# Optimization experiments

Measured on AMD Instinct MI355X. Metric: run time of the kernel, lower is better.

The kernel has to match this reference:

```python
import jax, jax.numpy as jnp
import numpy as np

B, S, H, M = 8, 128, 768, 128
EPS = 1e-12


def setup_inputs() -> dict:
    key = jax.random.key(0)
    ks = jax.random.split(key, 8)
    seq_hiddens = jax.random.normal(ks[0], (B, S, H), dtype=jnp.float32)
    gamma = jnp.ones((H,), jnp.float32)
    beta = jnp.zeros((H,), jnp.float32)
    # conditional LN dense weights (torch Linear weight: (out, in)); small init so math stays stable
    w_beta = jax.random.normal(ks[1], (H, H), dtype=jnp.float32) * 0.02
    w_gamma = jax.random.normal(ks[2], (H, H), dtype=jnp.float32) * 0.02
    w_ent = jax.random.normal(ks[3], (H, M), dtype=jnp.float32) * 0.02
    w_head = jax.random.normal(ks[4], (H, M), dtype=jnp.float32) * 0.02
    w_tail = jax.random.normal(ks[5], (H, M), dtype=jnp.float32) * 0.02
    b_ent = jnp.zeros((M,), jnp.float32)
    b_head = jnp.zeros((M,), jnp.float32)
    b_tail = jnp.zeros((M,), jnp.float32)
    return dict(seq_hiddens=seq_hiddens, gamma=gamma, beta=beta, w_beta=w_beta,
                w_gamma=w_gamma, w_ent=w_ent, b_ent=b_ent, w_head=w_head,
                b_head=b_head, w_tail=w_tail, b_tail=b_tail)


def _handshake_cln(seq, gamma, beta, w_beta, w_gamma):
    # Triangular pair expansion in the same row-major order as the torch loop:
    # for ind in range(S): pairs (ind, ind), (ind, ind+1), ..., (ind, S-1)
    s = seq.shape[1]
    ii, jj = jnp.triu_indices(s)                 # (P,) each, P = S(S+1)/2
    x = seq[:, jj, :]                            # visible hiddens   (B, P, H)
    cond = seq[:, ii, :]                         # repeated hiddens  (B, P, H)
    beta_c = jnp.einsum('bph,oh->bpo', cond, w_beta) + beta      # (B, P, H)
    gamma_c = jnp.einsum('bph,oh->bpo', cond, w_gamma) + gamma   # (B, P, H)
    mean = jnp.mean(x, axis=-1, keepdims=True)
    out = x - mean
    var = jnp.mean(out * out, axis=-1, keepdims=True)
    std = (var + EPS) ** 2                       # NOTE: faithful to source (no sqrt)
    return out / std * gamma_c + beta_c


def reference(seq_hiddens, gamma, beta, w_beta, w_gamma, w_ent, b_ent,
              w_head, b_head, w_tail, b_tail):
    shaking = _handshake_cln(seq_hiddens, gamma, beta, w_beta, w_gamma)  # (B, P, H)
    ent = jnp.tanh(shaking @ w_ent + b_ent)      # (B, P, M)
    head = jnp.tanh(shaking @ w_head + b_head)
    tail = jnp.tanh(shaking @ w_tail + b_tail)
    return jnp.stack([ent, head, tail], axis=0)  # (3, B, P, M)
```

## Files before the change

kernel.cpp:

```cpp
#include <hip/hip_runtime.h>
#include <hip/hip_bf16.h>
#include <hip/hip_fp16.h>
#include <math.h>

#define B_   8
#define S_   128
#define H_   768
#define M_   128
#define P_   8256
#define BP_  66048
#define EPSF 1e-12f

typedef unsigned short u16;
typedef unsigned int   u32;
typedef _Float16 h16;
typedef _Float16 ffrag __attribute__((ext_vector_type(8)));
typedef float    f32x4 __attribute__((ext_vector_type(4)));

__device__ __forceinline__ u32 fuse2(u32 x, u32 g, u32 b) {
    __half2 r = __hfma2(__builtin_bit_cast(__half2, x),
                        __builtin_bit_cast(__half2, g),
                        __builtin_bit_cast(__half2, b));
    return __builtin_bit_cast(u32, r);
}
__device__ __forceinline__ float fast_tanh(float v) {
    float t = __expf(v + v);
    float r = __builtin_amdgcn_rcpf(t + 1.0f);
    return fmaf(-2.0f, r, 1.0f);
}
__device__ __forceinline__ void gl_lds16(const h16* g, h16* l) {
    __builtin_amdgcn_global_load_lds(
        (const __attribute__((address_space(1))) u32*)g,
        (__attribute__((address_space(3))) u32*)l, 16, 0, 0);
}

#define NORM0 5763
__global__ void k_prep(const float* __restrict__ seq,
                       const float* __restrict__ wg, const float* __restrict__ wb,
                       const float* __restrict__ we, const float* __restrict__ wh,
                       const float* __restrict__ wt,
                       const float* __restrict__ be, const float* __restrict__ bh,
                       const float* __restrict__ bt,
                       h16* __restrict__ wgb, h16* __restrict__ wbb,
                       h16* __restrict__ wpk, float* __restrict__ biasc,
                       h16* __restrict__ xn, h16* __restrict__ condb)
{
    __shared__ float red[4];
    const int bx = blockIdx.x;
    const int t = threadIdx.x;

    if (bx < NORM0) {
        int idx = bx * 256 + t;
        if (idx < 589824) {
            wgb[idx] = (h16)wg[idx];
        } else if (idx < 1179648) {
            int i = idx - 589824;
            wbb[i] = (h16)wb[i];
        } else if (idx < 1474560) {
            int i = idx - 1179648;
            int e  = i & 7;
            int n  = (i >> 3) & 127;
            int v  = i >> 10;
            int ch = v & 7;
            int w2 = v >> 3;
            int kt = w2 % 12;
            int nb = w2 / 12;
            int h  = kt * 64 + ch * 8 + e;
            const float* src = (nb == 0) ? we : (nb == 1 ? wh : wt);
            wpk[i] = (h16)src[h * 128 + n];
        } else if (idx < 1474944) {
            int n = idx - 1474560;
            biasc[n] = (n < 128) ? be[n] : (n < 256 ? bh[n - 128] : bt[n - 256]);
        }
        return;
    }
    const int row = bx - NORM0;
    const int lane = t & 63, wid = t >> 6;
    const float* x = seq + (size_t)row * H_;
    float x0 = x[t], x1 = x[t + 256], x2 = x[t + 512];

    float s = x0 + x1 + x2;
    for (int o = 32; o; o >>= 1) s += __shfl_xor(s, o);
    if (lane == 0) red[wid] = s;
    __syncthreads();
    float mean = (red[0] + red[1] + red[2] + red[3]) * (1.0f / 768.0f);

    float c0 = x0 - mean, c1 = x1 - mean, c2 = x2 - mean;
    float ss = c0 * c0 + c1 * c1 + c2 * c2;
    for (int o = 32; o; o >>= 1) ss += __shfl_xor(ss, o);
    __syncthreads();
    if (lane == 0) red[wid] = ss;
    __syncthreads();
    float var = (red[0] + red[1] + red[2] + red[3]) * (1.0f / 768.0f);
    float sd = var + EPSF;
    float scale = 1.0f / (sd * sd);

    h16* xr = xn + (size_t)row * H_;
    h16* cr = condb + (size_t)row * H_;
    xr[t] = (h16)(c0 * scale); xr[t + 256] = (h16)(c1 * scale); xr[t + 512] = (h16)(c2 * scale);
    cr[t] = (h16)x0;           cr[t + 256] = (h16)x1;           cr[t + 512] = (h16)x2;
}

__global__ __launch_bounds__(256) void k_cond_gemm(
    const h16* __restrict__ Ab, const h16* __restrict__ Wg, const h16* __restrict__ Wb,
    const float* __restrict__ gamma, const float* __restrict__ beta,
    h16* __restrict__ Gc, h16* __restrict__ Bc)
{
    __shared__ h16 Ash[64 * 72];
    __shared__ h16 Bsh[64 * 72];
    const int t = threadIdx.x;
    const int row0 = blockIdx.x * 64;
    const int by = blockIdx.y;
    const bool isg = (by < 12);
    const int nc0 = (isg ? by : by - 12) * 64;
    const h16* wsrc = isg ? Wg : Wb;

    const int r = t >> 2, q = t & 3;
    const h16* ap = Ab + (size_t)(row0 + r) * H_ + q * 16;
    const h16* wp = wsrc + (size_t)(nc0 + r) * H_ + q * 16;
    h16* asto = &Ash[r * 72 + q * 16];
    h16* bsto = &Bsh[r * 72 + q * 16];

    const int lane = t & 63, wid = t >> 6;
    const int wm0 = (wid >> 1) * 32, wn0 = (wid & 1) * 32;
    const int l15 = lane & 15, quad = lane >> 4, q8 = quad * 8;

    f32x4 acc[2][2] = {};
    for (int kt = 0; kt < 12; ++kt) {
        const int k0 = kt * 64;
        uint4 a0 = *(const uint4*)(ap + k0); uint4 a1 = *(const uint4*)(ap + k0 + 8);
        uint4 w0 = *(const uint4*)(wp + k0); uint4 w1 = *(const uint4*)(wp + k0 + 8);
        *(uint4*)asto = a0; *(uint4*)(asto + 8) = a1;
        *(uint4*)bsto = w0; *(uint4*)(bsto + 8) = w1;
        __syncthreads();
#pragma unroll
        for (int ks = 0; ks < 64; ks += 32) {
            ffrag af[2], bf[2];
#pragma unroll
            for (int mi = 0; mi < 2; ++mi)
                af[mi] = *reinterpret_cast<const ffrag*>(&Ash[(wm0 + mi * 16 + l15) * 72 + ks + q8]);
#pragma unroll
            for (int ni = 0; ni < 2; ++ni)
                bf[ni] = *reinterpret_cast<const ffrag*>(&Bsh[(wn0 + ni * 16 + l15) * 72 + ks + q8]);
#pragma unroll
            for (int mi = 0; mi < 2; ++mi)
#pragma unroll
                for (int ni = 0; ni < 2; ++ni)
                    acc[mi][ni] = __builtin_amdgcn_mfma_f32_16x16x32_f16(af[mi], bf[ni], acc[mi][ni], 0, 0, 0);
        }
        __syncthreads();
    }

    const float* bias = isg ? gamma : beta;
    h16* outp = isg ? Gc : Bc;
#pragma unroll
    for (int mi = 0; mi < 2; ++mi)
#pragma unroll
        for (int ni = 0; ni < 2; ++ni) {
            int c = wn0 + ni * 16 + l15;
            float bv = bias[nc0 + c];
#pragma unroll
            for (int reg = 0; reg < 4; ++reg) {
                int rg = wm0 + mi * 16 + quad * 4 + reg;
                outp[(size_t)(row0 + rg) * H_ + nc0 + c] = (h16)(acc[mi][ni][reg] + bv);
            }
        }
}

__global__ __launch_bounds__(256, 2) void k_pair_gemm(
    const h16* __restrict__ Xn, const h16* __restrict__ Gcb, const h16* __restrict__ Bcb,
    const h16* __restrict__ Wpk, const float* __restrict__ biasc,
    float* __restrict__ out)
{
    __shared__ h16 Ash[2][8 * 128 * 8];
    __shared__ h16 Bsh[2][8 * 128 * 8];

    const int t = threadIdx.x;
    const int row0 = blockIdx.x * 128;
    const int nb = blockIdx.y;

    const int r_s = t >> 1, half = t & 1;
    int gp = row0 + r_s;
    int b = gp / P_;
    int p = gp - b * P_;
    int i = (int)((257.0f - sqrtf(66049.0f - 8.0f * (float)p)) * 0.5f);
    if (i < 0) i = 0; if (i > 127) i = 127;
    while (i > 0 && (i * (257 - i)) / 2 > p) --i;
    while (((i + 1) * (256 - i)) / 2 <= p) ++i;
    int j = i + (p - (i * (257 - i)) / 2);

    const h16* xp  = Xn  + (size_t)(b * 128 + j) * H_ + half * 32;
    const h16* gp_ = Gcb + (size_t)(b * 128 + i) * H_ + half * 32;
    const h16* bp_ = Bcb + (size_t)(b * 128 + i) * H_ + half * 32;
    int aw[4];
#pragma unroll
    for (int u = 0; u < 4; ++u)
        aw[u] = ((half * 4 + u) * 128 + r_s) * 8;

    const h16* wtile = Wpk + (size_t)nb * 12 * 8192;
    const int wud = t & ~63;

    const int lane = t & 63, wid = t >> 6;
    const int wm0 = (wid >> 1) * 64, wn0 = (wid & 1) * 64;
    const int l15 = lane & 15, quad = lane >> 4;

#pragma unroll
    for (int c = 0; c < 4; ++c)
        gl_lds16(wtile + (size_t)(c * 256 + t) * 8, &Bsh[0][(c * 256 + wud) * 8]);
    {
        uint4 xa[4], ga[4], ba[4];
#pragma unroll
        for (int u = 0; u < 4; ++u) {
            xa[u] = *(const uint4*)(xp + u * 8);
            ga[u] = *(const uint4*)(gp_ + u * 8);
            ba[u] = *(const uint4*)(bp_ + u * 8);
        }
#pragma unroll
        for (int u = 0; u < 4; ++u) {
            uint4 f;
            f.x = fuse2(xa[u].x, ga[u].x, ba[u].x); f.y = fuse2(xa[u].y, ga[u].y, ba[u].y);
            f.z = fuse2(xa[u].z, ga[u].z, ba[u].z); f.w = fuse2(xa[u].w, ga[u].w, ba[u].w);
            *(uint4*)&Ash[0][aw[u]] = f;
        }
    }
    __syncthreads();

    f32x4 acc[4][4] = {};
#pragma unroll 2
    for (int kt = 0; kt < 12; ++kt) {
        const int buf = kt & 1, nbf = buf ^ 1;
        uint4 xa[4], ga[4], ba[4];
        if (kt < 11) {
            const h16* wnext = wtile + (size_t)(kt + 1) * 8192;
#pragma unroll
            for (int c = 0; c < 4; ++c)
                gl_lds16(wnext + (size_t)(c * 256 + t) * 8, &Bsh[nbf][(c * 256 + wud) * 8]);
            const int k0 = (kt + 1) * 64;
#pragma unroll
            for (int u = 0; u < 4; ++u) {
                xa[u] = *(const uint4*)(xp + k0 + u * 8);
                ga[u] = *(const uint4*)(gp_ + k0 + u * 8);
                ba[u] = *(const uint4*)(bp_ + k0 + u * 8);
            }
        }

#pragma unroll
        for (int ks = 0; ks < 64; ks += 32) {
            const int ch0 = ks >> 3;
            ffrag af[4], bf[4];
#pragma unroll
            for (int mi = 0; mi < 4; ++mi)
                af[mi] = *reinterpret_cast<const ffrag*>(
                    &Ash[buf][((ch0 + quad) * 128 + wm0 + mi * 16 + l15) * 8]);
#pragma unroll
            for (int ni = 0; ni < 4; ++ni)
                bf[ni] = *reinterpret_cast<const ffrag*>(
                    &Bsh[buf][((ch0 + quad) * 128 + wn0 + ni * 16 + l15) * 8]);
#pragma unroll
            for (int mi = 0; mi < 4; ++mi)
#pragma unroll
                for (int ni = 0; ni < 4; ++ni)
                    acc[mi][ni] = __builtin_amdgcn_mfma_f32_16x16x32_f16(af[mi], bf[ni], acc[mi][ni], 0, 0, 0);
        }

        if (kt < 11) {
#pragma unroll
            for (int u = 0; u < 4; ++u) {
                uint4 f;
                f.x = fuse2(xa[u].x, ga[u].x, ba[u].x); f.y = fuse2(xa[u].y, ga[u].y, ba[u].y);
                f.z = fuse2(xa[u].z, ga[u].z, ba[u].z); f.w = fuse2(xa[u].w, ga[u].w, ba[u].w);
                *(uint4*)&Ash[nbf][aw[u]] = f;
            }
        }
        __syncthreads();
    }

#pragma unroll
    for (int mi = 0; mi < 4; ++mi)
#pragma unroll
        for (int ni = 0; ni < 4; ++ni) {
            int c = wn0 + ni * 16 + l15;
            float bv = biasc[nb * 128 + c];
#pragma unroll
            for (int reg = 0; reg < 4; ++reg) {
                int rg = wm0 + mi * 16 + quad * 4 + reg;
                out[((size_t)nb * BP_ + row0 + rg) * M_ + c] = fast_tanh(acc[mi][ni][reg] + bv);
            }
        }
}

extern "C" void kernel_launch(void* const* d_in, const int* in_sizes, int n_in,
                              void* d_out, int out_size, void* d_ws, size_t ws_size,
                              hipStream_t stream)
{
    const float* seq     = (const float*)d_in[0];
    const float* gamma   = (const float*)d_in[1];
    const float* beta    = (const float*)d_in[2];
    const float* w_beta  = (const float*)d_in[3];
    const float* w_gamma = (const float*)d_in[4];
    const float* w_ent   = (const float*)d_in[5];
    const float* b_ent   = (const float*)d_in[6];
    const float* w_head  = (const float*)d_in[7];
    const float* b_head  = (const float*)d_in[8];
    const float* w_tail  = (const float*)d_in[9];
    const float* b_tail  = (const float*)d_in[10];
    float* out = (float*)d_out;

    char* ws = (char*)d_ws;
    h16* xn    = (h16*)ws; ws += (size_t)1024 * 768 * 2;
    h16* condb = (h16*)ws; ws += (size_t)1024 * 768 * 2;
    h16* wgb   = (h16*)ws; ws += (size_t)768 * 768 * 2;
    h16* wbb   = (h16*)ws; ws += (size_t)768 * 768 * 2;
    h16* wpk   = (h16*)ws; ws += (size_t)294912 * 2;
    h16* gc    = (h16*)ws; ws += (size_t)1024 * 768 * 2;
    h16* bc    = (h16*)ws; ws += (size_t)1024 * 768 * 2;
    float* biasc = (float*)ws; ws += 384 * 4;

    hipLaunchKernelGGL(k_prep, dim3(NORM0 + 1024), dim3(256), 0, stream,
                       seq, w_gamma, w_beta, w_ent, w_head, w_tail,
                       b_ent, b_head, b_tail, wgb, wbb, wpk, biasc, xn, condb);
    hipLaunchKernelGGL(k_cond_gemm, dim3(16, 24), dim3(256), 0, stream,
                       condb, wgb, wbb, gamma, beta, gc, bc);
    hipLaunchKernelGGL(k_pair_gemm, dim3(516, 3), dim3(256), 0, stream,
                       xn, gc, bc, wpk, biasc, out);
}
```

Baseline: 200.5 us.

## Triple-buffer weight tiles and prefetch activations two stages ahead

The weight tile in shared memory becomes a three-slot ring, so the global-to-LDS copy for stage kt+2 is issued while stage kt is being multiplied. The fused activation tile for the next stage is now written to LDS before the MFMA block. Its register loads run two stages ahead, which gives global latency more time to hide. The full __syncthreads is replaced by an LDS-count wait plus s_barrier, and sched_barrier and setprio hints are added around the MFMA section. LDS per block grows to 80KB, which may limit occupancy. The lighter barrier relies on the compiler to insert the vector-memory waits for the asynchronous LDS copies.

```diff
diff --git a/kernel.cpp b/kernel.cpp
--- a/kernel.cpp
+++ b/kernel.cpp
@@ -173,7 +173,7 @@
     float* __restrict__ out)
 {
     __shared__ h16 Ash[2][8 * 128 * 8];
-    __shared__ h16 Bsh[2][8 * 128 * 8];
+    __shared__ h16 Bsh[3][8 * 128 * 8];
 
     const int t = threadIdx.x;
     const int row0 = blockIdx.x * 128;
@@ -204,38 +204,59 @@
     const int wm0 = (wid >> 1) * 64, wn0 = (wid & 1) * 64;
     const int l15 = lane & 15, quad = lane >> 4;
 
+    uint4 xa[4], ga[4], ba[4];
+
+#pragma unroll
+    for (int u = 0; u < 4; ++u) {
+        xa[u] = *(const uint4*)(xp + u * 8);
+        ga[u] = *(const uint4*)(gp_ + u * 8);
+        ba[u] = *(const uint4*)(bp_ + u * 8);
+    }
+#pragma unroll
+    for (int u = 0; u < 4; ++u) {
+        uint4 f;
+        f.x = fuse2(xa[u].x, ga[u].x, ba[u].x); f.y = fuse2(xa[u].y, ga[u].y, ba[u].y);
+        f.z = fuse2(xa[u].z, ga[u].z, ba[u].z); f.w = fuse2(xa[u].w, ga[u].w, ba[u].w);
+        *(uint4*)&Ash[0][aw[u]] = f;
+    }
 #pragma unroll
     for (int c = 0; c < 4; ++c)
         gl_lds16(wtile + (size_t)(c * 256 + t) * 8, &Bsh[0][(c * 256 + wud) * 8]);
-    {
-        uint4 xa[4], ga[4], ba[4];
-#pragma unroll
-        for (int u = 0; u < 4; ++u) {
-            xa[u] = *(const uint4*)(xp + u * 8);
-            ga[u] = *(const uint4*)(gp_ + u * 8);
-            ba[u] = *(const uint4*)(bp_ + u * 8);
-        }
-#pragma unroll
-        for (int u = 0; u < 4; ++u) {
-            uint4 f;
-            f.x = fuse2(xa[u].x, ga[u].x, ba[u].x); f.y = fuse2(xa[u].y, ga[u].y, ba[u].y);
-            f.z = fuse2(xa[u].z, ga[u].z, ba[u].z); f.w = fuse2(xa[u].w, ga[u].w, ba[u].w);
-            *(uint4*)&Ash[0][aw[u]] = f;
-        }
-    }
-    __syncthreads();
+#pragma unroll
+    for (int c = 0; c < 4; ++c)
+        gl_lds16(wtile + 8192 + (size_t)(c * 256 + t) * 8, &Bsh[1][(c * 256 + wud) * 8]);
+    __builtin_amdgcn_sched_barrier(0);
+#pragma unroll
+    for (int u = 0; u < 4; ++u) {
+        xa[u] = *(const uint4*)(xp + 64 + u * 8);
+        ga[u] = *(const uint4*)(gp_ + 64 + u * 8);
+        ba[u] = *(const uint4*)(bp_ + 64 + u * 8);
+    }
+    asm volatile("s_waitcnt lgkmcnt(0)" ::: "memory");
+    __builtin_amdgcn_s_barrier();
 
     f32x4 acc[4][4] = {};
-#pragma unroll 2
+    int bcur = 0, bpre = 2;
     for (int kt = 0; kt < 12; ++kt) {
-        const int buf = kt & 1, nbf = buf ^ 1;
-        uint4 xa[4], ga[4], ba[4];
+        if (kt < 10) {
+            const h16* wnext = wtile + (size_t)(kt + 2) * 8192;
+#pragma unroll
+            for (int c = 0; c < 4; ++c)
+                gl_lds16(wnext + (size_t)(c * 256 + t) * 8, &Bsh[bpre][(c * 256 + wud) * 8]);
+        }
+        __builtin_amdgcn_sched_barrier(0);
         if (kt < 11) {
-            const h16* wnext = wtile + (size_t)(kt + 1) * 8192;
-#pragma unroll
-            for (int c = 0; c < 4; ++c)
-                gl_lds16(wnext + (size_t)(c * 256 + t) * 8, &Bsh[nbf][(c * 256 + wud) * 8]);
-            const int k0 = (kt + 1) * 64;
+            const int abn = (kt + 1) & 1;
+#pragma unroll
+            for (int u = 0; u < 4; ++u) {
+                uint4 f;
+                f.x = fuse2(xa[u].x, ga[u].x, ba[u].x); f.y = fuse2(xa[u].y, ga[u].y, ba[u].y);
+                f.z = fuse2(xa[u].z, ga[u].z, ba[u].z); f.w = fuse2(xa[u].w, ga[u].w, ba[u].w);
+                *(uint4*)&Ash[abn][aw[u]] = f;
+            }
+        }
+        if (kt < 10) {
+            const int k0 = (kt + 2) * 64;
 #pragma unroll
             for (int u = 0; u < 4; ++u) {
                 xa[u] = *(const uint4*)(xp + k0 + u * 8);
@@ -243,36 +264,36 @@
                 ba[u] = *(const uint4*)(bp_ + k0 + u * 8);
             }
         }
-
-#pragma unroll
-        for (int ks = 0; ks < 64; ks += 32) {
-            const int ch0 = ks >> 3;
-            ffrag af[4], bf[4];
-#pragma unroll
-            for (int mi = 0; mi < 4; ++mi)
-                af[mi] = *reinterpret_cast<const ffrag*>(
-                    &Ash[buf][((ch0 + quad) * 128 + wm0 + mi * 16 + l15) * 8]);
-#pragma unroll
-            for (int ni = 0; ni < 4; ++ni)
-                bf[ni] = *reinterpret_cast<const ffrag*>(
-                    &Bsh[buf][((ch0 + quad) * 128 + wn0 + ni * 16 + l15) * 8]);
-#pragma unroll
-            for (int mi = 0; mi < 4; ++mi)
+        __builtin_amdgcn_sched_barrier(0);
+        {
+            const int ab = kt & 1;
+            __builtin_amdgcn_s_setprio(1);
+#pragma unroll
+            for (int ks = 0; ks < 64; ks += 32) {
+                const int ch0 = ks >> 3;
+                ffrag af[4], bf[4];
+#pragma unroll
+                for (int mi = 0; mi < 4; ++mi)
+                    af[mi] = *reinterpret_cast<const ffrag*>(
+                        &Ash[ab][((ch0 + quad) * 128 + wm0 + mi * 16 + l15) * 8]);
 #pragma unroll
                 for (int ni = 0; ni < 4; ++ni)
-                    acc[mi][ni] = __builtin_amdgcn_mfma_f32_16x16x32_f16(af[mi], bf[ni], acc[mi][ni], 0, 0, 0);
-        }
-
+                    bf[ni] = *reinterpret_cast<const ffrag*>(
+                        &Bsh[bcur][((ch0 + quad) * 128 + wn0 + ni * 16 + l15) * 8]);
+#pragma unroll
+                for (int mi = 0; mi < 4; ++mi)
+#pragma unroll
+                    for (int ni = 0; ni < 4; ++ni)
+                        acc[mi][ni] = __builtin_amdgcn_mfma_f32_16x16x32_f16(af[mi], bf[ni], acc[mi][ni], 0, 0, 0);
+            }
+            __builtin_amdgcn_s_setprio(0);
+        }
+        bcur = (bcur == 2) ? 0 : bcur + 1;
+        bpre = (bpre == 2) ? 0 : bpre + 1;
         if (kt < 11) {
-#pragma unroll
-            for (int u = 0; u < 4; ++u) {
-                uint4 f;
-                f.x = fuse2(xa[u].x, ga[u].x, ba[u].x); f.y = fuse2(xa[u].y, ga[u].y, ba[u].y);
-                f.z = fuse2(xa[u].z, ga[u].z, ba[u].z); f.w = fuse2(xa[u].w, ga[u].w, ba[u].w);
-                *(uint4*)&Ash[nbf][aw[u]] = f;
-            }
-        }
-        __syncthreads();
+            asm volatile("s_waitcnt lgkmcnt(0)" ::: "memory");
+            __builtin_amdgcn_s_barrier();
+        }
     }
 
 #pragma unroll
```

Measured after the change: 204.1 us. Within noise of the previous version (+1.8%).

## Switch pair GEMM to 32x32x16 MFMA with 32-wide K tiles and higher occupancy

Applied to the files above, without the earlier changes.

The main pair GEMM now uses 32x32x16 MFMA instructions instead of 16x16x32. The K tile drops from 64 to 32, so the loop runs 24 steps instead of 12, and launch bounds rise to 4 blocks per CU. The packed weight layout and LDS buffers are resized to match. The aim is fewer LDS fragment reads per FLOP and more resident waves to hide latency, at the cost of twice as many barriers and more per-step overhead in the K loop.

```diff
diff --git a/kernel.cpp b/kernel.cpp
--- a/kernel.cpp
+++ b/kernel.cpp
@@ -15,7 +15,7 @@
 typedef unsigned int   u32;
 typedef _Float16 h16;
 typedef _Float16 ffrag __attribute__((ext_vector_type(8)));
-typedef float    f32x4 __attribute__((ext_vector_type(4)));
+typedef float    f32x16 __attribute__((ext_vector_type(16)));
 
 __device__ __forceinline__ u32 fuse2(u32 x, u32 g, u32 b) {
     __half2 r = __hfma2(__builtin_bit_cast(__half2, x),
@@ -61,11 +61,11 @@
             int e  = i & 7;
             int n  = (i >> 3) & 127;
             int v  = i >> 10;
-            int ch = v & 7;
-            int w2 = v >> 3;
-            int kt = w2 % 12;
-            int nb = w2 / 12;
-            int h  = kt * 64 + ch * 8 + e;
+            int ch = v & 3;
+            int w2 = v >> 2;
+            int kt = w2 % 24;
+            int nb = w2 / 24;
+            int h  = kt * 32 + ch * 8 + e;
             const float* src = (nb == 0) ? we : (nb == 1 ? wh : wt);
             wpk[i] = (h16)src[h * 128 + n];
         } else if (idx < 1474944) {
@@ -125,6 +125,7 @@
     const int wm0 = (wid >> 1) * 32, wn0 = (wid & 1) * 32;
     const int l15 = lane & 15, quad = lane >> 4, q8 = quad * 8;
 
+    typedef float f32x4 __attribute__((ext_vector_type(4)));
     f32x4 acc[2][2] = {};
     for (int kt = 0; kt < 12; ++kt) {
         const int k0 = kt * 64;
@@ -167,13 +168,13 @@
         }
 }
 
-__global__ __launch_bounds__(256, 2) void k_pair_gemm(
+__global__ __launch_bounds__(256, 4) void k_pair_gemm(
     const h16* __restrict__ Xn, const h16* __restrict__ Gcb, const h16* __restrict__ Bcb,
     const h16* __restrict__ Wpk, const float* __restrict__ biasc,
     float* __restrict__ out)
 {
-    __shared__ h16 Ash[2][8 * 128 * 8];
-    __shared__ h16 Bsh[2][8 * 128 * 8];
+    __shared__ h16 Ash[2][4 * 128 * 8];
+    __shared__ h16 Bsh[2][4 * 128 * 8];
 
     const int t = threadIdx.x;
     const int row0 = blockIdx.x * 128;
@@ -189,101 +190,90 @@
     while (((i + 1) * (256 - i)) / 2 <= p) ++i;
     int j = i + (p - (i * (257 - i)) / 2);
 
-    const h16* xp  = Xn  + (size_t)(b * 128 + j) * H_ + half * 32;
-    const h16* gp_ = Gcb + (size_t)(b * 128 + i) * H_ + half * 32;
-    const h16* bp_ = Bcb + (size_t)(b * 128 + i) * H_ + half * 32;
-    int aw[4];
-#pragma unroll
-    for (int u = 0; u < 4; ++u)
-        aw[u] = ((half * 4 + u) * 128 + r_s) * 8;
-
-    const h16* wtile = Wpk + (size_t)nb * 12 * 8192;
+    const h16* xp  = Xn  + (size_t)(b * 128 + j) * H_ + half * 16;
+    const h16* gp_ = Gcb + (size_t)(b * 128 + i) * H_ + half * 16;
+    const h16* bp_ = Bcb + (size_t)(b * 128 + i) * H_ + half * 16;
+    const int aw0 = ((half * 2 + 0) * 128 + r_s) * 8;
+    const int aw1 = ((half * 2 + 1) * 128 + r_s) * 8;
+
+    const h16* wtile = Wpk + (size_t)nb * 24 * 4096;
     const int wud = t & ~63;
 
     const int lane = t & 63, wid = t >> 6;
     const int wm0 = (wid >> 1) * 64, wn0 = (wid & 1) * 64;
-    const int l15 = lane & 15, quad = lane >> 4;
-
-#pragma unroll
-    for (int c = 0; c < 4; ++c)
+    const int l31 = lane & 31, hi = lane >> 5;
+
+#pragma unroll
+    for (int c = 0; c < 2; ++c)
         gl_lds16(wtile + (size_t)(c * 256 + t) * 8, &Bsh[0][(c * 256 + wud) * 8]);
     {
-        uint4 xa[4], ga[4], ba[4];
-#pragma unroll
-        for (int u = 0; u < 4; ++u) {
-            xa[u] = *(const uint4*)(xp + u * 8);
-            ga[u] = *(const uint4*)(gp_ + u * 8);
-            ba[u] = *(const uint4*)(bp_ + u * 8);
-        }
-#pragma unroll
-        for (int u = 0; u < 4; ++u) {
-            uint4 f;
-            f.x = fuse2(xa[u].x, ga[u].x, ba[u].x); f.y = fuse2(xa[u].y, ga[u].y, ba[u].y);
-            f.z = fuse2(xa[u].z, ga[u].z, ba[u].z); f.w = fuse2(xa[u].w, ga[u].w, ba[u].w);
-            *(uint4*)&Ash[0][aw[u]] = f;
-        }
+        uint4 xa0 = *(const uint4*)xp;       uint4 xa1 = *(const uint4*)(xp + 8);
+        uint4 ga0 = *(const uint4*)gp_;      uint4 ga1 = *(const uint4*)(gp_ + 8);
+        uint4 ba0 = *(const uint4*)bp_;      uint4 ba1 = *(const uint4*)(bp_ + 8);
+        uint4 f0, f1;
+        f0.x = fuse2(xa0.x, ga0.x, ba0.x); f0.y = fuse2(xa0.y, ga0.y, ba0.y);
+        f0.z = fuse2(xa0.z, ga0.z, ba0.z); f0.w = fuse2(xa0.w, ga0.w, ba0.w);
+        f1.x = fuse2(xa1.x, ga1.x, ba1.x); f1.y = fuse2(xa1.y, ga1.y, ba1.y);
+        f1.z = fuse2(xa1.z, ga1.z, ba1.z); f1.w = fuse2(xa1.w, ga1.w, ba1.w);
+        *(uint4*)&Ash[0][aw0] = f0; *(uint4*)&Ash[0][aw1] = f1;
     }
     __syncthreads();
 
-    f32x4 acc[4][4] = {};
+    f32x16 acc[2][2] = {};
 #pragma unroll 2
-    for (int kt = 0; kt < 12; ++kt) {
+    for (int kt = 0; kt < 24; ++kt) {
         const int buf = kt & 1, nbf = buf ^ 1;
-        uint4 xa[4], ga[4], ba[4];
-        if (kt < 11) {
-            const h16* wnext = wtile + (size_t)(kt + 1) * 8192;
-#pragma unroll
-            for (int c = 0; c < 4; ++c)
+        uint4 xa0, xa1, ga0, ga1, ba0, ba1;
+        if (kt < 23) {
+            const h16* wnext = wtile + (size_t)(kt + 1) * 4096;
+#pragma unroll
+            for (int c = 0; c < 2; ++c)
                 gl_lds16(wnext + (size_t)(c * 256 + t) * 8, &Bsh[nbf][(c * 256 + wud) * 8]);
-            const int k0 = (kt + 1) * 64;
-#pragma unroll
-            for (int u = 0; u < 4; ++u) {
-                xa[u] = *(const uint4*)(xp + k0 + u * 8);
-                ga[u] = *(const uint4*)(gp_ + k0 + u * 8);
-                ba[u] = *(const uint4*)(bp_ + k0 + u * 8);
-            }
-        }
-
-#pragma unroll
-        for (int ks = 0; ks < 64; ks += 32) {
-            const int ch0 = ks >> 3;
-            ffrag af[4], bf[4];
-#pragma unroll
-            for (int mi = 0; mi < 4; ++mi)
+            const int k0 = (kt + 1) * 32;
+            xa0 = *(const uint4*)(xp + k0);  xa1 = *(const uint4*)(xp + k0 + 8);
+            ga0 = *(const uint4*)(gp_ + k0); ga1 = *(const uint4*)(gp_ + k0 + 8);
+            ba0 = *(const uint4*)(bp_ + k0); ba1 = *(const uint4*)(bp_ + k0 + 8);
+        }
+
+#pragma unroll
+        for (int ks = 0; ks < 2; ++ks) {
+            const int ch0 = ks * 2;
+            ffrag af[2], bf[2];
+#pragma unroll
+            for (int mi = 0; mi < 2; ++mi)
                 af[mi] = *reinterpret_cast<const ffrag*>(
-                    &Ash[buf][((ch0 + quad) * 128 + wm0 + mi * 16 + l15) * 8]);
-#pragma unroll
-            for (int ni = 0; ni < 4; ++ni)
+                    &Ash[buf][((ch0 + hi) * 128 + wm0 + mi * 32 + l31) * 8]);
+#pragma unroll
+            for (int ni = 0; ni < 2; ++ni)
                 bf[ni] = *reinterpret_cast<const ffrag*>(
-                    &Bsh[buf][((ch0 + quad) * 128 + wn0 + ni * 16 + l15) * 8]);
-#pragma unroll
-            for (int mi = 0; mi < 4; ++mi)
-#pragma unroll
-                for (int ni = 0; ni < 4; ++ni)
-                    acc[mi][ni] = __builtin_amdgcn_mfma_f32_16x16x32_f16(af[mi], bf[ni], acc[mi][ni], 0, 0, 0);
-        }
-
-        if (kt < 11) {
-#pragma unroll
-            for (int u = 0; u < 4; ++u) {
-                uint4 f;
-                f.x = fuse2(xa[u].x, ga[u].x, ba[u].x); f.y = fuse2(xa[u].y, ga[u].y, ba[u].y);
-                f.z = fuse2(xa[u].z, ga[u].z, ba[u].z); f.w = fuse2(xa[u].w, ga[u].w, ba[u].w);
-                *(uint4*)&Ash[nbf][aw[u]] = f;
-            }
+                    &Bsh[buf][((ch0 + hi) * 128 + wn0 + ni * 32 + l31) * 8]);
+#pragma unroll
+            for (int mi = 0; mi < 2; ++mi)
+#pragma unroll
+                for (int ni = 0; ni < 2; ++ni)
+                    acc[mi][ni] = __builtin_amdgcn_mfma_f32_32x32x16_f16(af[mi], bf[ni], acc[mi][ni], 0, 0, 0);
+        }
+
+        if (kt < 23) {
+            uint4 f0, f1;
+            f0.x = fuse2(xa0.x, ga0.x, ba0.x); f0.y = fuse2(xa0.y, ga0.y, ba0.y);
+            f0.z = fuse2(xa0.z, ga0.z, ba0.z); f0.w = fuse2(xa0.w, ga0.w, ba0.w);
+            f1.x = fuse2(xa1.x, ga1.x, ba1.x); f1.y = fuse2(xa1.y, ga1.y, ba1.y);
+            f1.z = fuse2(xa1.z, ga1.z, ba1.z); f1.w = fuse2(xa1.w, ga1.w, ba1.w);
+            *(uint4*)&Ash[nbf][aw0] = f0; *(uint4*)&Ash[nbf][aw1] = f1;
         }
         __syncthreads();
     }
 
 #pragma unroll
-    for (int mi = 0; mi < 4; ++mi)
-#pragma unroll
-        for (int ni = 0; ni < 4; ++ni) {
-            int c = wn0 + ni * 16 + l15;
+    for (int mi = 0; mi < 2; ++mi)
+#pragma unroll
+        for (int ni = 0; ni < 2; ++ni) {
+            int c = wn0 + ni * 32 + l31;
             float bv = biasc[nb * 128 + c];
 #pragma unroll
-            for (int reg = 0; reg < 4; ++reg) {
-                int rg = wm0 + mi * 16 + quad * 4 + reg;
+            for (int reg = 0; reg < 16; ++reg) {
+                int rg = wm0 + mi * 32 + (reg & 3) + 8 * (reg >> 2) + 4 * hi;
                 out[((size_t)nb * BP_ + row0 + rg) * M_ + c] = fast_tanh(acc[mi][ni][reg] + bv);
             }
         }
```

Result: no change. 198.2 us (-1.1%).
